# Kernel tuning notes

Measured on AMD Instinct MI355X. Metric: run time of the kernel, lower is better.

Reference implementation:

```python
import jax, jax.numpy as jnp
import numpy as np

DIM = 1024
HEADS = 8
NUM_KEYS = 256
TOPK = 32
D_HEAD = DIM // HEADS
BATCH = 2
SEQ = 2048


def setup_inputs() -> dict:
    key = jax.random.key(0)
    ks = jax.random.split(key, 5)
    x = jax.random.normal(ks[0], (BATCH, SEQ, DIM), jnp.float32)
    # nn.Linear(dim, 2*dim, bias=False): weight (2*dim, dim)
    Wq = jax.random.normal(ks[1], (2 * DIM, DIM), jnp.float32) * (DIM ** -0.5)
    # nn.Parameter(torch.randn(heads, num_keys, 2, d_head))
    keys = jax.random.normal(ks[2], (HEADS, NUM_KEYS, 2, D_HEAD), jnp.float32)
    # nn.Parameter(torch.randn(heads, num_keys**2, d_head))
    values = jax.random.normal(ks[3], (HEADS, NUM_KEYS ** 2, D_HEAD), jnp.float32)
    # nn.Linear(dim, dim): weight (dim, dim), bias (dim,)
    Wo = jax.random.normal(ks[4], (DIM, DIM), jnp.float32) * (DIM ** -0.5)
    bo = jnp.zeros((DIM,), jnp.float32)
    return {"x": x, "Wq": Wq, "keys": keys, "values": values, "Wo": Wo, "bo": bo}


def reference(x, Wq, keys, values, Wo, bo):
    b, t, e = x.shape
    h, dh, k, nk = HEADS, D_HEAD, TOPK, NUM_KEYS
    # to_queries + chunk(2, dim=-1) + stack -> (2, b, t, h, d_head)
    q = x @ Wq.T                                    # (b, t, 2*dim)
    q = q.reshape(b, t, 2, e).transpose(2, 0, 1, 3)  # (2, b, t, dim), matches chunk+stack
    q = q.reshape(2, b, t, h, dh)
    # dual sub-key scores: (b, h, t, 2, num_keys)
    dots = jnp.einsum('pbthd,hnpd->bhtpn', q, keys)
    # top-k over num_keys per sub-key
    scores, indices = jax.lax.top_k(dots, k)         # (b, h, t, 2, k)
    # faithful to source: chunk(2, dim=2) splits the TIME axis
    th = t // 2
    s0, s1 = scores[:, :, :th], scores[:, :, th:]
    i0, i1 = indices[:, :, :th], indices[:, :, th:]
    # Cartesian combination: (b, h, t//2, 2, k, k) -> (b, h, t, k*k)
    all_scores = (s0[..., :, None] + s1[..., None, :]).reshape(b, h, t, k * k)
    all_indices = (i0[..., :, None] * nk + i1[..., None, :]).reshape(b, h, t, k * k)
    # final top-k over the k^2 candidates
    final_scores, final_idx = jax.lax.top_k(all_scores, k)   # (b, h, t, k)
    value_indices = jnp.take_along_axis(all_indices, final_idx, axis=-1)  # (b, h, t, k)
    attn = jax.nn.softmax(final_scores, axis=-1)
    # gather values per head: values (h, nk^2, dh), idx (b, h, t, k) -> (b, h, t, k, dh)
    sel = jax.vmap(lambda v, idx: v[idx], in_axes=(0, 1), out_axes=1)(values, value_indices)
    out = jnp.einsum('bhtk,bhtkd->bhtd', attn, sel)  # weighted sum over top-k
    out = out.transpose(0, 2, 1, 3).reshape(b, t, e)
    return out @ Wo.T + bo
```

## Files before the change

kernel.cpp:

```cpp
#include <hip/hip_runtime.h>

typedef unsigned int u32;
typedef unsigned long long u64;
typedef _Float16 f16;
typedef __attribute__((ext_vector_type(4))) _Float16 f16x4;
typedef __attribute__((ext_vector_type(8))) _Float16 f16x8;
typedef __attribute__((ext_vector_type(4))) float f32x4;
typedef const __attribute__((address_space(1))) void* gp_t;
typedef __attribute__((address_space(3))) void* lp_t;

#define TSEQ 2048

__device__ __forceinline__ u32 f2sort(float f) {
  u32 u = __float_as_uint(f);
  return u ^ ((u32)((int)u >> 31) | 0x80000000u);
}
__device__ __forceinline__ float sort2f(u32 u) {
  u ^= (u & 0x80000000u) ? 0x80000000u : 0xFFFFFFFFu;
  return __uint_as_float(u);
}

__device__ __forceinline__ void glds16(const f16* g, f16* l) {
  __builtin_amdgcn_global_load_lds((gp_t)g, (lp_t)l, 16, 0, 0);
}

__device__ __forceinline__ u32 umax2(u32 a, u32 b) { return a > b ? a : b; }

__device__ __forceinline__ u32 dppmax16(u32 v) {
  u32 t;
  t = (u32)__builtin_amdgcn_update_dpp(0, (int)v, 0x128, 0xF, 0xF, true);
  v = v > t ? v : t;
  t = (u32)__builtin_amdgcn_update_dpp(0, (int)v, 0x124, 0xF, 0xF, true);
  v = v > t ? v : t;
  t = (u32)__builtin_amdgcn_update_dpp(0, (int)v, 0x122, 0xF, 0xF, true);
  v = v > t ? v : t;
  t = (u32)__builtin_amdgcn_update_dpp(0, (int)v, 0x121, 0xF, 0xF, true);
  v = v > t ? v : t;
  return v;
}
__device__ __forceinline__ float dppsum16(float v) {
  float t;
  t = __int_as_float(
      __builtin_amdgcn_update_dpp(0, __float_as_int(v), 0x128, 0xF, 0xF, true));
  v += t;
  t = __int_as_float(
      __builtin_amdgcn_update_dpp(0, __float_as_int(v), 0x124, 0xF, 0xF, true));
  v += t;
  t = __int_as_float(
      __builtin_amdgcn_update_dpp(0, __float_as_int(v), 0x122, 0xF, 0xF, true));
  v += t;
  t = __int_as_float(
      __builtin_amdgcn_update_dpp(0, __float_as_int(v), 0x121, 0xF, 0xF, true));
  v += t;
  return v;
}

__device__ __forceinline__ u32 tree16(const u32* k) {
  u32 t0 = umax2(k[0], k[1]), t1 = umax2(k[2], k[3]);
  u32 t2 = umax2(k[4], k[5]), t3 = umax2(k[6], k[7]);
  u32 t4 = umax2(k[8], k[9]), t5 = umax2(k[10], k[11]);
  u32 t6 = umax2(k[12], k[13]), t7 = umax2(k[14], k[15]);
  t0 = umax2(t0, t1); t2 = umax2(t2, t3);
  t4 = umax2(t4, t5); t6 = umax2(t6, t7);
  return umax2(umax2(t0, t2), umax2(t4, t6));
}

__global__ __launch_bounds__(256) void cvt_all(
    const float* __restrict__ x, const float* __restrict__ wq,
    const float* __restrict__ wo, const float* __restrict__ ky,
    f16* __restrict__ xd, f16* __restrict__ wqd, f16* __restrict__ wod,
    f16* __restrict__ kyd) {
  int g = blockIdx.x * 256 + threadIdx.x;
  const float* s;
  f16* d;
  int off;
  if (g < 1048576)      { s = x;  d = xd;  off = g; }
  else if (g < 1572864) { s = wq; d = wqd; off = g - 1048576; }
  else if (g < 1835008) { s = wo; d = wod; off = g - 1572864; }
  else                  { s = ky; d = kyd; off = g - 1835008; }
  float4 v = ((const float4*)s)[off];
  f16x4 o;
  o[0] = (f16)v.x; o[1] = (f16)v.y; o[2] = (f16)v.z; o[3] = (f16)v.w;
  ((f16x4*)d)[off] = o;
}

template <int BN>
__global__ __launch_bounds__(256) void gemm_f16(
    const f16* __restrict__ A, int lda, const f16* __restrict__ B, int ldb,
    const float* __restrict__ bias, void* __restrict__ Cv, int ldc, int K,
    int c_f16) {
  constexpr int NJ = BN / 32;
  __shared__ f16 As[128 * 32];
  __shared__ f16 Bs[BN * 32];
  const int tid = threadIdx.x;
  const int lane = tid & 63, wave = tid >> 6;
  const int m0 = blockIdx.y << 7, n0 = blockIdx.x * BN;
  const int c0 = wave * 128 + lane, c1 = c0 + 64;
  const int r0 = c0 >> 2, s0 = c0 & 3;
  const int r1 = c1 >> 2, s1 = c1 & 3;
  const int cB = wave * 64 + lane;
  const int rB = cB >> 2, sB = cB & 3;
  const f16* Ab = A + (size_t)m0 * lda;
  const f16* Bb = B + (size_t)n0 * ldb;
  const int fm = lane & 15, fq = lane >> 4, fk = fq << 3;
  const int wm = (wave >> 1) << 6, wn = (wave & 1) * (BN / 2);
  f32x4 acc[4][NJ] = {};
  for (int k0 = 0; k0 < K; k0 += 32) {
    __syncthreads();
    glds16(Ab + (size_t)r0 * lda + k0 + s0 * 8, As + (size_t)c0 * 8 - lane * 8);
    glds16(Ab + (size_t)r1 * lda + k0 + s1 * 8, As + (size_t)c1 * 8 - lane * 8);
    if constexpr (BN == 128) {
      glds16(Bb + (size_t)r0 * ldb + k0 + s0 * 8,
             Bs + (size_t)c0 * 8 - lane * 8);
      glds16(Bb + (size_t)r1 * ldb + k0 + s1 * 8,
             Bs + (size_t)c1 * 8 - lane * 8);
    } else {
      glds16(Bb + (size_t)rB * ldb + k0 + sB * 8,
             Bs + (size_t)cB * 8 - lane * 8);
    }
    __syncthreads();
    f16x8 af[4], bf[NJ];
#pragma unroll
    for (int mi = 0; mi < 4; mi++)
      af[mi] = *(const f16x8*)&As[(wm + mi * 16 + fm) * 32 + fk];
#pragma unroll
    for (int nj = 0; nj < NJ; nj++)
      bf[nj] = *(const f16x8*)&Bs[(wn + nj * 16 + fm) * 32 + fk];
#pragma unroll
    for (int mi = 0; mi < 4; mi++)
#pragma unroll
      for (int nj = 0; nj < NJ; nj++)
        acc[mi][nj] = __builtin_amdgcn_mfma_f32_16x16x32_f16(
            af[mi], bf[nj], acc[mi][nj], 0, 0, 0);
  }
  if (c_f16) {
    f16* C = (f16*)Cv;
#pragma unroll
    for (int mi = 0; mi < 4; mi++)
#pragma unroll
      for (int r = 0; r < 4; r++) {
        int row = m0 + wm + mi * 16 + fq * 4 + r;
        f16* cp = C + (size_t)row * ldc + n0 + wn + fm;
#pragma unroll
        for (int nj = 0; nj < NJ; nj++) cp[nj * 16] = (f16)acc[mi][nj][r];
      }
  } else {
    float* C = (float*)Cv;
    float bb[NJ];
#pragma unroll
    for (int nj = 0; nj < NJ; nj++)
      bb[nj] = bias ? bias[n0 + wn + nj * 16 + fm] : 0.f;
#pragma unroll
    for (int mi = 0; mi < 4; mi++)
#pragma unroll
      for (int r = 0; r < 4; r++) {
        int row = m0 + wm + mi * 16 + fq * 4 + r;
        float* cp = C + (size_t)row * ldc + n0 + wn + fm;
#pragma unroll
        for (int nj = 0; nj < NJ; nj++) cp[nj * 16] = acc[mi][nj][r] + bb[nj];
      }
  }
}

__global__ __launch_bounds__(256) void dots_topk1(
    const f16* __restrict__ Q,
    const f16* __restrict__ keysf,
    float* __restrict__ s1s, int* __restrict__ s1i) {
  __shared__ f16 As[64 * 32];
  __shared__ f16 Bs[256 * 32];
  const int tid = threadIdx.x;
  const int lane = tid & 63, wave = tid >> 6;
  const int z = blockIdx.x;
  const int h = z >> 1, p = z & 1;
  const int m0 = blockIdx.y << 6;
  const f16* Aq = Q + (size_t)m0 * 2048 + p * 1024 + h * 128;
  const f16* Bk = keysf + ((size_t)h * 512 + p) * 128;
  const int cA = wave * 64 + lane;
  const int rA = cA >> 2, sA = cA & 3;
  const int fm = lane & 15, fq = lane >> 4, fk = fq << 3;
  f32x4 acc[16] = {};
  for (int k0 = 0; k0 < 128; k0 += 32) {
    __syncthreads();
    glds16(Aq + (size_t)rA * 2048 + k0 + sA * 8, As + (size_t)cA * 8 - lane * 8);
#pragma unroll
    for (int c = 0; c < 4; c++) {
      int cB = (wave * 4 + c) * 64 + lane;
      int rB = cB >> 2, sB = cB & 3;
      glds16(Bk + (size_t)rB * 256 + k0 + sB * 8,
             Bs + (size_t)cB * 8 - lane * 8);
    }
    __syncthreads();
    f16x8 af = *(const f16x8*)&As[(wave * 16 + fm) * 32 + fk];
#pragma unroll
    for (int j = 0; j < 16; j++) {
      f16x8 bf = *(const f16x8*)&Bs[(j * 16 + fm) * 32 + fk];
      acc[j] = __builtin_amdgcn_mfma_f32_16x16x32_f16(af, bf, acc[j], 0, 0, 0);
    }
  }
#pragma unroll
  for (int rp = 0; rp < 2; rp++) {
    u32 keyA[16], keyB[16];
#pragma unroll
    for (int j = 0; j < 16; j++) {
      keyA[j] = (f2sort(acc[j][2 * rp]) & ~0xFFu) | (u32)((j << 4) | fm);
      keyB[j] = (f2sort(acc[j][2 * rp + 1]) & ~0xFFu) | (u32)((j << 4) | fm);
    }
    u32 g0A = 0, g1A = 0, g0B = 0, g1B = 0;
    for (int it = 0; it < 32; it++) {
      u32 lmA = tree16(keyA);
      u32 lmB = tree16(keyB);
      u32 gmA = dppmax16(lmA);
      u32 gmB = dppmax16(lmB);
#pragma unroll
      for (int j = 0; j < 16; j++) {
        keyA[j] = (keyA[j] == gmA) ? 0u : keyA[j];
        keyB[j] = (keyB[j] == gmB) ? 0u : keyB[j];
      }
      bool sel = (fm == (it & 15));
      if (it < 16) {
        g0A = sel ? gmA : g0A;
        g0B = sel ? gmB : g0B;
      } else {
        g1A = sel ? gmA : g1A;
        g1B = sel ? gmB : g1B;
      }
    }
    int mA = m0 + wave * 16 + (fq << 2) + 2 * rp;
    int bA = mA >> 11, tA = mA & 2047;
    size_t orowA = ((((size_t)(bA * 8 + h)) * TSEQ + tA) * 2 + p) * 32;
    s1s[orowA + fm] = sort2f(g0A & ~0xFFu);
    s1s[orowA + fm + 16] = sort2f(g1A & ~0xFFu);
    s1i[orowA + fm] = (int)(g0A & 0xFFu);
    s1i[orowA + fm + 16] = (int)(g1A & 0xFFu);
    int mB = mA + 1;
    int bB = mB >> 11, tB = mB & 2047;
    size_t orowB = ((((size_t)(bB * 8 + h)) * TSEQ + tB) * 2 + p) * 32;
    s1s[orowB + fm] = sort2f(g0B & ~0xFFu);
    s1s[orowB + fm + 16] = sort2f(g1B & ~0xFFu);
    s1i[orowB + fm] = (int)(g0B & 0xFFu);
    s1i[orowB + fm + 16] = (int)(g1B & 0xFFu);
  }
}

__global__ __launch_bounds__(256) void topk2_gather(
    const float* __restrict__ s1s, const int* __restrict__ s1i,
    const float* __restrict__ valf, f16* __restrict__ headout) {
  __shared__ unsigned short cand[128];
  __shared__ float s0sh[16][32];
  __shared__ float s1sh[16][32];
  __shared__ int i0sh[16][32];
  __shared__ int i1sh[16][32];
  __shared__ int vtab[16][32];
  __shared__ float wtab[16][32];
  const int tid = threadIdx.x;
  if (tid < 128) {
    int c = tid;
    unsigned short enc = 0xFFFF;
    if (c < 119) {
      int rem = c, i = 0;
      for (i = 0; i < 32; i++) {
        int cnt = 32 / (i + 1);
        if (rem < cnt) break;
        rem -= cnt;
      }
      enc = (unsigned short)((i << 5) | rem);
    }
    cand[tid] = enc;
  }
  __syncthreads();
  const int rloc = tid >> 4;
  const int l = tid & 15;
  for (int g = 0; g < 4; g++) {
    const int grp = g * 512 + blockIdx.x;
    const int row = grp * 16 + rloc;
    const int b = row >> 14;
    const int h = (row >> 11) & 7;
    const int t = row & 2047;
    const int tt = t >> 1, p = t & 1;
    size_t rbase = (size_t)(b * 8 + h) * TSEQ;
    size_t base0 = ((rbase + tt) * 2 + p) * 32;
    size_t base1 = ((rbase + tt + 1024) * 2 + p) * 32;
    s0sh[rloc][l] = s1s[base0 + l];
    s0sh[rloc][l + 16] = s1s[base0 + l + 16];
    s1sh[rloc][l] = s1s[base1 + l];
    s1sh[rloc][l + 16] = s1s[base1 + l + 16];
    i0sh[rloc][l] = s1i[base0 + l];
    i0sh[rloc][l + 16] = s1i[base0 + l + 16];
    i1sh[rloc][l] = s1i[base1 + l];
    i1sh[rloc][l + 16] = s1i[base1 + l + 16];
    u32 key[8];
#pragma unroll
    for (int s = 0; s < 8; s++) {
      int c = l + 16 * s;
      unsigned short e = cand[c];
      u32 kk = 0u;
      if (e != 0xFFFF) {
        float v = s0sh[rloc][e >> 5] + s1sh[rloc][e & 31];
        kk = (f2sort(v) & ~0xFFu) | (u32)c;
      }
      key[s] = kk;
    }
    u32 g0 = 0, g1 = 0;
    for (int it = 0; it < 32; it++) {
      u32 t0 = umax2(key[0], key[1]), t1 = umax2(key[2], key[3]);
      u32 t2 = umax2(key[4], key[5]), t3 = umax2(key[6], key[7]);
      u32 lm = umax2(umax2(t0, t1), umax2(t2, t3));
      u32 gm = dppmax16(lm);
#pragma unroll
      for (int s = 0; s < 8; s++) key[s] = (key[s] == gm) ? 0u : key[s];
      bool sel = (l == (it & 15));
      if (it < 16) g0 = sel ? gm : g0;
      else         g1 = sel ? gm : g1;
    }
    float sc0 = sort2f(g0 & ~0xFFu);
    float sc1 = sort2f(g1 & ~0xFFu);
    unsigned short e0c = cand[g0 & 0xFFu];
    unsigned short e1c = cand[g1 & 0xFFu];
    int vidx0 = i0sh[rloc][e0c >> 5] * 256 + i1sh[rloc][e0c & 31];
    int vidx1 = i0sh[rloc][e1c >> 5] * 256 + i1sh[rloc][e1c & 31];
    float mx = __int_as_float(
        __builtin_amdgcn_ds_swizzle(__float_as_int(sc0), 0x010));
    float e0 = __expf(sc0 - mx);
    float e1 = __expf(sc1 - mx);
    float inv = 1.0f / dppsum16(e0 + e1);
    vtab[rloc][l] = vidx0;
    vtab[rloc][l + 16] = vidx1;
    wtab[rloc][l] = e0 * inv;
    wtab[rloc][l + 16] = e1 * inv;
    const float* vb = valf + (((size_t)h) << 23) + (size_t)l * 8;
    float accf[8] = {};
#pragma unroll 8
    for (int k = 0; k < 32; k++) {
      int vi = vtab[rloc][k];
      float wk = wtab[rloc][k];
      const float4* vp = (const float4*)(vb + (size_t)vi * 128);
      float4 v0 = vp[0];
      float4 v1 = vp[1];
      accf[0] += wk * v0.x; accf[1] += wk * v0.y;
      accf[2] += wk * v0.z; accf[3] += wk * v0.w;
      accf[4] += wk * v1.x; accf[5] += wk * v1.y;
      accf[6] += wk * v1.z; accf[7] += wk * v1.w;
    }
    f16x8 o;
#pragma unroll
    for (int j = 0; j < 8; j++) o[j] = (f16)accf[j];
    f16* op = headout + (size_t)(b * TSEQ + t) * 1024 + h * 128 + l * 8;
    *(f16x8*)op = o;
  }
}

extern "C" void kernel_launch(void* const* d_in, const int* in_sizes, int n_in,
                              void* d_out, int out_size, void* d_ws,
                              size_t ws_size, hipStream_t stream) {
  const float* x    = (const float*)d_in[0];
  const float* Wq   = (const float*)d_in[1];
  const float* keys = (const float*)d_in[2];
  const float* vals = (const float*)d_in[3];
  const float* Wo   = (const float*)d_in[4];
  const float* bo   = (const float*)d_in[5];
  float* out = (float*)d_out;
  char* ws = (char*)d_ws;
  f16*   xf   = (f16*)(ws);
  f16*   wqf  = (f16*)(ws + (size_t)(8u << 20));
  f16*   wof  = (f16*)(ws + (size_t)(12u << 20));
  f16*   kyf  = (f16*)(ws + (size_t)(14u << 20));
  f16*   Qf   = (f16*)(ws + (size_t)(16u << 20));
  float* s1s  = (float*)(ws + (size_t)(32u << 20));
  int*   s1i  = (int*)(ws + (size_t)(40u << 20));
  f16*   hof  = (f16*)(ws + (size_t)(48u << 20));

  cvt_all<<<dim3(7680), 256, 0, stream>>>(x, Wq, Wo, keys, xf, wqf, wof, kyf);
  gemm_f16<128><<<dim3(16, 32), 256, 0, stream>>>(xf, 1024, wqf, 1024, nullptr,
                                                  Qf, 2048, 1024, 1);
  dots_topk1<<<dim3(16, 64), 256, 0, stream>>>(Qf, kyf, s1s, s1i);
  topk2_gather<<<dim3(512), 256, 0, stream>>>(s1s, s1i, vals, hof);
  gemm_f16<64><<<dim3(16, 32), 256, 0, stream>>>(hof, 1024, wof, 1024, bo, out,
                                                 1024, 1024, 0);
}
```

Baseline: 535.6 us.

## Fuse query projection GEMM into sub-key dot top-k kernel; flatten gather grid

Measured after the change: 550.6 us. 2.8% more time.

```diff
diff --git a/kernel.cpp b/kernel.cpp
--- a/kernel.cpp
+++ b/kernel.cpp
@@ -162,38 +162,67 @@
   }
 }
 
-__global__ __launch_bounds__(256) void dots_topk1(
-    const f16* __restrict__ Q,
+__global__ __launch_bounds__(256) void qdots_topk1(
+    const f16* __restrict__ xf,
+    const f16* __restrict__ wqf,
     const f16* __restrict__ keysf,
     float* __restrict__ s1s, int* __restrict__ s1i) {
-  __shared__ f16 As[64 * 32];
-  __shared__ f16 Bs[256 * 32];
+  __shared__ f16 Axs[64 * 64];
+  __shared__ f16 Bws[128 * 64];
+  __shared__ f16 Qs[4][64 * 32];
   const int tid = threadIdx.x;
   const int lane = tid & 63, wave = tid >> 6;
   const int z = blockIdx.x;
   const int h = z >> 1, p = z & 1;
   const int m0 = blockIdx.y << 6;
-  const f16* Aq = Q + (size_t)m0 * 2048 + p * 1024 + h * 128;
+  const int nbase = p * 1024 + h * 128;
+  const int fm = lane & 15, fq = lane >> 4, fk = fq << 3;
+  f32x4 accQ[8] = {};
+  for (int k0 = 0; k0 < 1024; k0 += 64) {
+    __syncthreads();
+    {
+      int c = tid;
+      glds16(xf + (size_t)(m0 + (c >> 3)) * 1024 + k0 + (c & 7) * 8,
+             Axs + (size_t)c * 8 - lane * 8);
+      c = tid + 256;
+      glds16(xf + (size_t)(m0 + (c >> 3)) * 1024 + k0 + (c & 7) * 8,
+             Axs + (size_t)c * 8 - lane * 8);
+    }
+#pragma unroll
+    for (int q = 0; q < 4; q++) {
+      int c = tid + 256 * q;
+      glds16(wqf + (size_t)(nbase + (c >> 3)) * 1024 + k0 + (c & 7) * 8,
+             Bws + (size_t)c * 8 - lane * 8);
+    }
+    __syncthreads();
+#pragma unroll
+    for (int s = 0; s < 2; s++) {
+      f16x8 af = *(const f16x8*)&Axs[(wave * 16 + fm) * 64 + s * 32 + fk];
+#pragma unroll
+      for (int j = 0; j < 8; j++) {
+        f16x8 bw = *(const f16x8*)&Bws[(j * 16 + fm) * 64 + s * 32 + fk];
+        accQ[j] =
+            __builtin_amdgcn_mfma_f32_16x16x32_f16(af, bw, accQ[j], 0, 0, 0);
+      }
+    }
+  }
+#pragma unroll
+  for (int j = 0; j < 8; j++) {
+    int pn = j >> 1;
+    int kk = (j & 1) * 16 + fm;
+#pragma unroll
+    for (int r = 0; r < 4; r++)
+      Qs[pn][(wave * 16 + fq * 4 + r) * 32 + kk] = (f16)accQ[j][r];
+  }
+  __syncthreads();
   const f16* Bk = keysf + ((size_t)h * 512 + p) * 128;
-  const int cA = wave * 64 + lane;
-  const int rA = cA >> 2, sA = cA & 3;
-  const int fm = lane & 15, fq = lane >> 4, fk = fq << 3;
   f32x4 acc[16] = {};
+#pragma unroll
   for (int k0 = 0; k0 < 128; k0 += 32) {
-    __syncthreads();
-    glds16(Aq + (size_t)rA * 2048 + k0 + sA * 8, As + (size_t)cA * 8 - lane * 8);
-#pragma unroll
-    for (int c = 0; c < 4; c++) {
-      int cB = (wave * 4 + c) * 64 + lane;
-      int rB = cB >> 2, sB = cB & 3;
-      glds16(Bk + (size_t)rB * 256 + k0 + sB * 8,
-             Bs + (size_t)cB * 8 - lane * 8);
-    }
-    __syncthreads();
-    f16x8 af = *(const f16x8*)&As[(wave * 16 + fm) * 32 + fk];
+    f16x8 af = *(const f16x8*)&Qs[k0 >> 5][(wave * 16 + fm) * 32 + fk];
 #pragma unroll
     for (int j = 0; j < 16; j++) {
-      f16x8 bf = *(const f16x8*)&Bs[(j * 16 + fm) * 32 + fk];
+      f16x8 bf = *(const f16x8*)&Bk[(size_t)(j * 16 + fm) * 256 + k0 + fk];
       acc[j] = __builtin_amdgcn_mfma_f32_16x16x32_f16(af, bf, acc[j], 0, 0, 0);
     }
   }
@@ -267,86 +296,83 @@
     }
     cand[tid] = enc;
   }
-  __syncthreads();
   const int rloc = tid >> 4;
   const int l = tid & 15;
-  for (int g = 0; g < 4; g++) {
-    const int grp = g * 512 + blockIdx.x;
-    const int row = grp * 16 + rloc;
-    const int b = row >> 14;
-    const int h = (row >> 11) & 7;
-    const int t = row & 2047;
-    const int tt = t >> 1, p = t & 1;
-    size_t rbase = (size_t)(b * 8 + h) * TSEQ;
-    size_t base0 = ((rbase + tt) * 2 + p) * 32;
-    size_t base1 = ((rbase + tt + 1024) * 2 + p) * 32;
-    s0sh[rloc][l] = s1s[base0 + l];
-    s0sh[rloc][l + 16] = s1s[base0 + l + 16];
-    s1sh[rloc][l] = s1s[base1 + l];
-    s1sh[rloc][l + 16] = s1s[base1 + l + 16];
-    i0sh[rloc][l] = s1i[base0 + l];
-    i0sh[rloc][l + 16] = s1i[base0 + l + 16];
-    i1sh[rloc][l] = s1i[base1 + l];
-    i1sh[rloc][l + 16] = s1i[base1 + l + 16];
-    u32 key[8];
-#pragma unroll
-    for (int s = 0; s < 8; s++) {
-      int c = l + 16 * s;
-      unsigned short e = cand[c];
-      u32 kk = 0u;
-      if (e != 0xFFFF) {
-        float v = s0sh[rloc][e >> 5] + s1sh[rloc][e & 31];
-        kk = (f2sort(v) & ~0xFFu) | (u32)c;
-      }
-      key[s] = kk;
-    }
-    u32 g0 = 0, g1 = 0;
-    for (int it = 0; it < 32; it++) {
-      u32 t0 = umax2(key[0], key[1]), t1 = umax2(key[2], key[3]);
-      u32 t2 = umax2(key[4], key[5]), t3 = umax2(key[6], key[7]);
-      u32 lm = umax2(umax2(t0, t1), umax2(t2, t3));
-      u32 gm = dppmax16(lm);
-#pragma unroll
-      for (int s = 0; s < 8; s++) key[s] = (key[s] == gm) ? 0u : key[s];
-      bool sel = (l == (it & 15));
-      if (it < 16) g0 = sel ? gm : g0;
-      else         g1 = sel ? gm : g1;
-    }
-    float sc0 = sort2f(g0 & ~0xFFu);
-    float sc1 = sort2f(g1 & ~0xFFu);
-    unsigned short e0c = cand[g0 & 0xFFu];
-    unsigned short e1c = cand[g1 & 0xFFu];
-    int vidx0 = i0sh[rloc][e0c >> 5] * 256 + i1sh[rloc][e0c & 31];
-    int vidx1 = i0sh[rloc][e1c >> 5] * 256 + i1sh[rloc][e1c & 31];
-    float mx = __int_as_float(
-        __builtin_amdgcn_ds_swizzle(__float_as_int(sc0), 0x010));
-    float e0 = __expf(sc0 - mx);
-    float e1 = __expf(sc1 - mx);
-    float inv = 1.0f / dppsum16(e0 + e1);
-    vtab[rloc][l] = vidx0;
-    vtab[rloc][l + 16] = vidx1;
-    wtab[rloc][l] = e0 * inv;
-    wtab[rloc][l + 16] = e1 * inv;
-    const float* vb = valf + (((size_t)h) << 23) + (size_t)l * 8;
-    float accf[8] = {};
+  const int row = blockIdx.x * 16 + rloc;
+  const int b = row >> 14;
+  const int h = (row >> 11) & 7;
+  const int t = row & 2047;
+  const int tt = t >> 1, p = t & 1;
+  size_t rbase = (size_t)(b * 8 + h) * TSEQ;
+  size_t base0 = ((rbase + tt) * 2 + p) * 32;
+  size_t base1 = ((rbase + tt + 1024) * 2 + p) * 32;
+  s0sh[rloc][l] = s1s[base0 + l];
+  s0sh[rloc][l + 16] = s1s[base0 + l + 16];
+  s1sh[rloc][l] = s1s[base1 + l];
+  s1sh[rloc][l + 16] = s1s[base1 + l + 16];
+  i0sh[rloc][l] = s1i[base0 + l];
+  i0sh[rloc][l + 16] = s1i[base0 + l + 16];
+  i1sh[rloc][l] = s1i[base1 + l];
+  i1sh[rloc][l + 16] = s1i[base1 + l + 16];
+  __syncthreads();
+  u32 key[8];
+#pragma unroll
+  for (int s = 0; s < 8; s++) {
+    int c = l + 16 * s;
+    unsigned short e = cand[c];
+    u32 kk = 0u;
+    if (e != 0xFFFF) {
+      float v = s0sh[rloc][e >> 5] + s1sh[rloc][e & 31];
+      kk = (f2sort(v) & ~0xFFu) | (u32)c;
+    }
+    key[s] = kk;
+  }
+  u32 g0 = 0, g1 = 0;
+  for (int it = 0; it < 32; it++) {
+    u32 t0 = umax2(key[0], key[1]), t1 = umax2(key[2], key[3]);
+    u32 t2 = umax2(key[4], key[5]), t3 = umax2(key[6], key[7]);
+    u32 lm = umax2(umax2(t0, t1), umax2(t2, t3));
+    u32 gm = dppmax16(lm);
+#pragma unroll
+    for (int s = 0; s < 8; s++) key[s] = (key[s] == gm) ? 0u : key[s];
+    bool sel = (l == (it & 15));
+    if (it < 16) g0 = sel ? gm : g0;
+    else         g1 = sel ? gm : g1;
+  }
+  float sc0 = sort2f(g0 & ~0xFFu);
+  float sc1 = sort2f(g1 & ~0xFFu);
+  unsigned short e0c = cand[g0 & 0xFFu];
+  unsigned short e1c = cand[g1 & 0xFFu];
+  int vidx0 = i0sh[rloc][e0c >> 5] * 256 + i1sh[rloc][e0c & 31];
+  int vidx1 = i0sh[rloc][e1c >> 5] * 256 + i1sh[rloc][e1c & 31];
+  float mx = __int_as_float(
+      __builtin_amdgcn_ds_swizzle(__float_as_int(sc0), 0x010));
+  float e0 = __expf(sc0 - mx);
+  float e1 = __expf(sc1 - mx);
+  float inv = 1.0f / dppsum16(e0 + e1);
+  vtab[rloc][l] = vidx0;
+  vtab[rloc][l + 16] = vidx1;
+  wtab[rloc][l] = e0 * inv;
+  wtab[rloc][l + 16] = e1 * inv;
+  const float* vb = valf + (((size_t)h) << 23) + (size_t)l * 8;
+  float accf[8] = {};
 #pragma unroll 8
-    for (int k = 0; k < 32; k++) {
-      int vi = vtab[rloc][k];
-      float wk = wtab[rloc][k];
-      const float4* vp = (const float4*)(vb + (size_t)vi * 128);
-      float4 v0 = vp[0];
-      float4 v1 = vp[1];
-      accf[0] += wk * v0.x; accf[1] += wk * v0.y;
-      accf[2] += wk * v0.z; accf[3] += wk * v0.w;
-      accf[4] += wk * v1.x; accf[5] += wk * v1.y;
-      accf[6] += wk * v1.z; accf[7] += wk * v1.w;
-    }
-    f16x8 o;
-#pragma unroll
-    for (int j = 0; j < 8; j++) o[j] = (f16)accf[j];
-    f16* op = headout + (size_t)(b * TSEQ + t) * 1024 + h * 128 + l * 8;
-    *(f16x8*)op = o;
-  }
+  for (int k = 0; k < 32; k++) {
+    int vi = vtab[rloc][k];
+    float wk = wtab[rloc][k];
+    const float4* vp = (const float4*)(vb + (size_t)vi * 128);
+    float4 v0 = vp[0];
+    float4 v1 = vp[1];
+    accf[0] += wk * v0.x; accf[1] += wk * v0.y;
+    accf[2] += wk * v0.z; accf[3] += wk * v0.w;
+    accf[4] += wk * v1.x; accf[5] += wk * v1.y;
+    accf[6] += wk * v1.z; accf[7] += wk * v1.w;
+  }
+  f16x8 o;
+#pragma unroll
+  for (int j = 0; j < 8; j++) o[j] = (f16)accf[j];
+  f16* op = headout + (size_t)(b * TSEQ + t) * 1024 + h * 128 + l * 8;
+  *(f16x8*)op = o;
 }
 
 extern "C" void kernel_launch(void* const* d_in, const int* in_sizes, int n_in,
@@ -364,16 +390,13 @@
   f16*   wqf  = (f16*)(ws + (size_t)(8u << 20));
   f16*   wof  = (f16*)(ws + (size_t)(12u << 20));
   f16*   kyf  = (f16*)(ws + (size_t)(14u << 20));
-  f16*   Qf   = (f16*)(ws + (size_t)(16u << 20));
-  float* s1s  = (float*)(ws + (size_t)(32u << 20));
-  int*   s1i  = (int*)(ws + (size_t)(40u << 20));
-  f16*   hof  = (f16*)(ws + (size_t)(48u << 20));
+  float* s1s  = (float*)(ws + (size_t)(16u << 20));
+  int*   s1i  = (int*)(ws + (size_t)(24u << 20));
+  f16*   hof  = (f16*)(ws + (size_t)(32u << 20));
 
   cvt_all<<<dim3(7680), 256, 0, stream>>>(x, Wq, Wo, keys, xf, wqf, wof, kyf);
-  gemm_f16<128><<<dim3(16, 32), 256, 0, stream>>>(xf, 1024, wqf, 1024, nullptr,
-                                                  Qf, 2048, 1024, 1);
-  dots_topk1<<<dim3(16, 64), 256, 0, stream>>>(Qf, kyf, s1s, s1i);
-  topk2_gather<<<dim3(512), 256, 0, stream>>>(s1s, s1i, vals, hof);
+  qdots_topk1<<<dim3(16, 64), 256, 0, stream>>>(xf, wqf, kyf, s1s, s1i);
+  topk2_gather<<<dim3(32768 / 16), 256, 0, stream>>>(s1s, s1i, vals, hof);
   gemm_f16<64><<<dim3(16, 32), 256, 0, stream>>>(hof, 1024, wof, 1024, bo, out,
                                                  1024, 1024, 0);
 }
```

## Double-buffer LDS tiles in GEMM and dots kernels; flatten topk2 grid

Applied to the files above, without the earlier changes.

After: 515.1 us. 1.04x faster.

```diff
diff --git a/kernel.cpp b/kernel.cpp
--- a/kernel.cpp
+++ b/kernel.cpp
@@ -22,6 +22,17 @@
 
 __device__ __forceinline__ void glds16(const f16* g, f16* l) {
   __builtin_amdgcn_global_load_lds((gp_t)g, (lp_t)l, 16, 0, 0);
+}
+
+template <int N> __device__ __forceinline__ void waitvm() {
+  if constexpr (N == 0) asm volatile("s_waitcnt vmcnt(0)" ::: "memory");
+  else if constexpr (N == 3) asm volatile("s_waitcnt vmcnt(3)" ::: "memory");
+  else if constexpr (N == 4) asm volatile("s_waitcnt vmcnt(4)" ::: "memory");
+  else asm volatile("s_waitcnt vmcnt(5)" ::: "memory");
+}
+__device__ __forceinline__ void barrier_fenced() {
+  __builtin_amdgcn_s_barrier();
+  __builtin_amdgcn_sched_barrier(0);
 }
 
 __device__ __forceinline__ u32 umax2(u32 a, u32 b) { return a > b ? a : b; }
@@ -90,8 +101,9 @@
     const float* __restrict__ bias, void* __restrict__ Cv, int ldc, int K,
     int c_f16) {
   constexpr int NJ = BN / 32;
-  __shared__ f16 As[128 * 32];
-  __shared__ f16 Bs[BN * 32];
+  constexpr int NLD = (BN == 128) ? 4 : 3;
+  __shared__ f16 As[2][128 * 32];
+  __shared__ f16 Bs[2][BN * 32];
   const int tid = threadIdx.x;
   const int lane = tid & 63, wave = tid >> 6;
   const int m0 = blockIdx.y << 7, n0 = blockIdx.x * BN;
@@ -105,33 +117,46 @@
   const int fm = lane & 15, fq = lane >> 4, fk = fq << 3;
   const int wm = (wave >> 1) << 6, wn = (wave & 1) * (BN / 2);
   f32x4 acc[4][NJ] = {};
-  for (int k0 = 0; k0 < K; k0 += 32) {
-    __syncthreads();
-    glds16(Ab + (size_t)r0 * lda + k0 + s0 * 8, As + (size_t)c0 * 8 - lane * 8);
-    glds16(Ab + (size_t)r1 * lda + k0 + s1 * 8, As + (size_t)c1 * 8 - lane * 8);
+  auto stage = [&](int buf, int k0) {
+    glds16(Ab + (size_t)r0 * lda + k0 + s0 * 8,
+           As[buf] + (size_t)c0 * 8 - lane * 8);
+    glds16(Ab + (size_t)r1 * lda + k0 + s1 * 8,
+           As[buf] + (size_t)c1 * 8 - lane * 8);
     if constexpr (BN == 128) {
       glds16(Bb + (size_t)r0 * ldb + k0 + s0 * 8,
-             Bs + (size_t)c0 * 8 - lane * 8);
+             Bs[buf] + (size_t)c0 * 8 - lane * 8);
       glds16(Bb + (size_t)r1 * ldb + k0 + s1 * 8,
-             Bs + (size_t)c1 * 8 - lane * 8);
+             Bs[buf] + (size_t)c1 * 8 - lane * 8);
     } else {
       glds16(Bb + (size_t)rB * ldb + k0 + sB * 8,
-             Bs + (size_t)cB * 8 - lane * 8);
-    }
-    __syncthreads();
+             Bs[buf] + (size_t)cB * 8 - lane * 8);
+    }
+  };
+  const int nt = K >> 5;
+  stage(0, 0);
+  for (int t = 0; t < nt; t++) {
+    const int cur = t & 1;
+    if (t + 1 < nt) {
+      stage(cur ^ 1, (t + 1) << 5);
+      waitvm<NLD>();
+    } else {
+      waitvm<0>();
+    }
+    barrier_fenced();
     f16x8 af[4], bf[NJ];
 #pragma unroll
     for (int mi = 0; mi < 4; mi++)
-      af[mi] = *(const f16x8*)&As[(wm + mi * 16 + fm) * 32 + fk];
+      af[mi] = *(const f16x8*)&As[cur][(wm + mi * 16 + fm) * 32 + fk];
 #pragma unroll
     for (int nj = 0; nj < NJ; nj++)
-      bf[nj] = *(const f16x8*)&Bs[(wn + nj * 16 + fm) * 32 + fk];
+      bf[nj] = *(const f16x8*)&Bs[cur][(wn + nj * 16 + fm) * 32 + fk];
 #pragma unroll
     for (int mi = 0; mi < 4; mi++)
 #pragma unroll
       for (int nj = 0; nj < NJ; nj++)
         acc[mi][nj] = __builtin_amdgcn_mfma_f32_16x16x32_f16(
             af[mi], bf[nj], acc[mi][nj], 0, 0, 0);
+    barrier_fenced();
   }
   if (c_f16) {
     f16* C = (f16*)Cv;
@@ -166,8 +191,8 @@
     const f16* __restrict__ Q,
     const f16* __restrict__ keysf,
     float* __restrict__ s1s, int* __restrict__ s1i) {
-  __shared__ f16 As[64 * 32];
-  __shared__ f16 Bs[256 * 32];
+  __shared__ f16 As[2][64 * 32];
+  __shared__ f16 Bs[2][256 * 32];
   const int tid = threadIdx.x;
   const int lane = tid & 63, wave = tid >> 6;
   const int z = blockIdx.x;
@@ -178,24 +203,35 @@
   const int cA = wave * 64 + lane;
   const int rA = cA >> 2, sA = cA & 3;
   const int fm = lane & 15, fq = lane >> 4, fk = fq << 3;
-  f32x4 acc[16] = {};
-  for (int k0 = 0; k0 < 128; k0 += 32) {
-    __syncthreads();
-    glds16(Aq + (size_t)rA * 2048 + k0 + sA * 8, As + (size_t)cA * 8 - lane * 8);
+  auto stage = [&](int buf, int k0) {
+    glds16(Aq + (size_t)rA * 2048 + k0 + sA * 8,
+           As[buf] + (size_t)cA * 8 - lane * 8);
 #pragma unroll
     for (int c = 0; c < 4; c++) {
       int cB = (wave * 4 + c) * 64 + lane;
       int rB = cB >> 2, sB = cB & 3;
       glds16(Bk + (size_t)rB * 256 + k0 + sB * 8,
-             Bs + (size_t)cB * 8 - lane * 8);
-    }
-    __syncthreads();
-    f16x8 af = *(const f16x8*)&As[(wave * 16 + fm) * 32 + fk];
+             Bs[buf] + (size_t)cB * 8 - lane * 8);
+    }
+  };
+  f32x4 acc[16] = {};
+  stage(0, 0);
+  for (int t = 0; t < 4; t++) {
+    const int cur = t & 1;
+    if (t < 3) {
+      stage(cur ^ 1, (t + 1) << 5);
+      waitvm<5>();
+    } else {
+      waitvm<0>();
+    }
+    barrier_fenced();
+    f16x8 af = *(const f16x8*)&As[cur][(wave * 16 + fm) * 32 + fk];
 #pragma unroll
     for (int j = 0; j < 16; j++) {
-      f16x8 bf = *(const f16x8*)&Bs[(j * 16 + fm) * 32 + fk];
+      f16x8 bf = *(const f16x8*)&Bs[cur][(j * 16 + fm) * 32 + fk];
       acc[j] = __builtin_amdgcn_mfma_f32_16x16x32_f16(af, bf, acc[j], 0, 0, 0);
     }
+    barrier_fenced();
   }
 #pragma unroll
   for (int rp = 0; rp < 2; rp++) {
@@ -267,86 +303,83 @@
     }
     cand[tid] = enc;
   }
-  __syncthreads();
   const int rloc = tid >> 4;
   const int l = tid & 15;
-  for (int g = 0; g < 4; g++) {
-    const int grp = g * 512 + blockIdx.x;
-    const int row = grp * 16 + rloc;
-    const int b = row >> 14;
-    const int h = (row >> 11) & 7;
-    const int t = row & 2047;
-    const int tt = t >> 1, p = t & 1;
-    size_t rbase = (size_t)(b * 8 + h) * TSEQ;
-    size_t base0 = ((rbase + tt) * 2 + p) * 32;
-    size_t base1 = ((rbase + tt + 1024) * 2 + p) * 32;
-    s0sh[rloc][l] = s1s[base0 + l];
-    s0sh[rloc][l + 16] = s1s[base0 + l + 16];
-    s1sh[rloc][l] = s1s[base1 + l];
-    s1sh[rloc][l + 16] = s1s[base1 + l + 16];
-    i0sh[rloc][l] = s1i[base0 + l];
-    i0sh[rloc][l + 16] = s1i[base0 + l + 16];
-    i1sh[rloc][l] = s1i[base1 + l];
-    i1sh[rloc][l + 16] = s1i[base1 + l + 16];
-    u32 key[8];
-#pragma unroll
-    for (int s = 0; s < 8; s++) {
-      int c = l + 16 * s;
-      unsigned short e = cand[c];
-      u32 kk = 0u;
-      if (e != 0xFFFF) {
-        float v = s0sh[rloc][e >> 5] + s1sh[rloc][e & 31];
-        kk = (f2sort(v) & ~0xFFu) | (u32)c;
-      }
-      key[s] = kk;
-    }
-    u32 g0 = 0, g1 = 0;
-    for (int it = 0; it < 32; it++) {
-      u32 t0 = umax2(key[0], key[1]), t1 = umax2(key[2], key[3]);
-      u32 t2 = umax2(key[4], key[5]), t3 = umax2(key[6], key[7]);
-      u32 lm = umax2(umax2(t0, t1), umax2(t2, t3));
-      u32 gm = dppmax16(lm);
-#pragma unroll
-      for (int s = 0; s < 8; s++) key[s] = (key[s] == gm) ? 0u : key[s];
-      bool sel = (l == (it & 15));
-      if (it < 16) g0 = sel ? gm : g0;
-      else         g1 = sel ? gm : g1;
-    }
-    float sc0 = sort2f(g0 & ~0xFFu);
-    float sc1 = sort2f(g1 & ~0xFFu);
-    unsigned short e0c = cand[g0 & 0xFFu];
-    unsigned short e1c = cand[g1 & 0xFFu];
-    int vidx0 = i0sh[rloc][e0c >> 5] * 256 + i1sh[rloc][e0c & 31];
-    int vidx1 = i0sh[rloc][e1c >> 5] * 256 + i1sh[rloc][e1c & 31];
-    float mx = __int_as_float(
-        __builtin_amdgcn_ds_swizzle(__float_as_int(sc0), 0x010));
-    float e0 = __expf(sc0 - mx);
-    float e1 = __expf(sc1 - mx);
-    float inv = 1.0f / dppsum16(e0 + e1);
-    vtab[rloc][l] = vidx0;
-    vtab[rloc][l + 16] = vidx1;
-    wtab[rloc][l] = e0 * inv;
-    wtab[rloc][l + 16] = e1 * inv;
-    const float* vb = valf + (((size_t)h) << 23) + (size_t)l * 8;
-    float accf[8] = {};
+  const int row = blockIdx.x * 16 + rloc;
+  const int b = row >> 14;
+  const int h = (row >> 11) & 7;
+  const int t = row & 2047;
+  const int tt = t >> 1, p = t & 1;
+  size_t rbase = (size_t)(b * 8 + h) * TSEQ;
+  size_t base0 = ((rbase + tt) * 2 + p) * 32;
+  size_t base1 = ((rbase + tt + 1024) * 2 + p) * 32;
+  s0sh[rloc][l] = s1s[base0 + l];
+  s0sh[rloc][l + 16] = s1s[base0 + l + 16];
+  s1sh[rloc][l] = s1s[base1 + l];
+  s1sh[rloc][l + 16] = s1s[base1 + l + 16];
+  i0sh[rloc][l] = s1i[base0 + l];
+  i0sh[rloc][l + 16] = s1i[base0 + l + 16];
+  i1sh[rloc][l] = s1i[base1 + l];
+  i1sh[rloc][l + 16] = s1i[base1 + l + 16];
+  __syncthreads();
+  u32 key[8];
+#pragma unroll
+  for (int s = 0; s < 8; s++) {
+    int c = l + 16 * s;
+    unsigned short e = cand[c];
+    u32 kk = 0u;
+    if (e != 0xFFFF) {
+      float v = s0sh[rloc][e >> 5] + s1sh[rloc][e & 31];
+      kk = (f2sort(v) & ~0xFFu) | (u32)c;
+    }
+    key[s] = kk;
+  }
+  u32 g0 = 0, g1 = 0;
+  for (int it = 0; it < 32; it++) {
+    u32 t0 = umax2(key[0], key[1]), t1 = umax2(key[2], key[3]);
+    u32 t2 = umax2(key[4], key[5]), t3 = umax2(key[6], key[7]);
+    u32 lm = umax2(umax2(t0, t1), umax2(t2, t3));
+    u32 gm = dppmax16(lm);
+#pragma unroll
+    for (int s = 0; s < 8; s++) key[s] = (key[s] == gm) ? 0u : key[s];
+    bool sel = (l == (it & 15));
+    if (it < 16) g0 = sel ? gm : g0;
+    else         g1 = sel ? gm : g1;
+  }
+  float sc0 = sort2f(g0 & ~0xFFu);
+  float sc1 = sort2f(g1 & ~0xFFu);
+  unsigned short e0c = cand[g0 & 0xFFu];
+  unsigned short e1c = cand[g1 & 0xFFu];
+  int vidx0 = i0sh[rloc][e0c >> 5] * 256 + i1sh[rloc][e0c & 31];
+  int vidx1 = i0sh[rloc][e1c >> 5] * 256 + i1sh[rloc][e1c & 31];
+  float mx = __int_as_float(
+      __builtin_amdgcn_ds_swizzle(__float_as_int(sc0), 0x010));
+  float e0 = __expf(sc0 - mx);
+  float e1 = __expf(sc1 - mx);
+  float inv = 1.0f / dppsum16(e0 + e1);
+  vtab[rloc][l] = vidx0;
+  vtab[rloc][l + 16] = vidx1;
+  wtab[rloc][l] = e0 * inv;
+  wtab[rloc][l + 16] = e1 * inv;
+  const float* vb = valf + (((size_t)h) << 23) + (size_t)l * 8;
+  float accf[8] = {};
 #pragma unroll 8
-    for (int k = 0; k < 32; k++) {
-      int vi = vtab[rloc][k];
-      float wk = wtab[rloc][k];
-      const float4* vp = (const float4*)(vb + (size_t)vi * 128);
-      float4 v0 = vp[0];
-      float4 v1 = vp[1];
-      accf[0] += wk * v0.x; accf[1] += wk * v0.y;
-      accf[2] += wk * v0.z; accf[3] += wk * v0.w;
-      accf[4] += wk * v1.x; accf[5] += wk * v1.y;
-      accf[6] += wk * v1.z; accf[7] += wk * v1.w;
-    }
-    f16x8 o;
-#pragma unroll
-    for (int j = 0; j < 8; j++) o[j] = (f16)accf[j];
-    f16* op = headout + (size_t)(b * TSEQ + t) * 1024 + h * 128 + l * 8;
-    *(f16x8*)op = o;
-  }
+  for (int k = 0; k < 32; k++) {
+    int vi = vtab[rloc][k];
+    float wk = wtab[rloc][k];
+    const float4* vp = (const float4*)(vb + (size_t)vi * 128);
+    float4 v0 = vp[0];
+    float4 v1 = vp[1];
+    accf[0] += wk * v0.x; accf[1] += wk * v0.y;
+    accf[2] += wk * v0.z; accf[3] += wk * v0.w;
+    accf[4] += wk * v1.x; accf[5] += wk * v1.y;
+    accf[6] += wk * v1.z; accf[7] += wk * v1.w;
+  }
+  f16x8 o;
+#pragma unroll
+  for (int j = 0; j < 8; j++) o[j] = (f16)accf[j];
+  f16* op = headout + (size_t)(b * TSEQ + t) * 1024 + h * 128 + l * 8;
+  *(f16x8*)op = o;
 }
 
 extern "C" void kernel_launch(void* const* d_in, const int* in_sizes, int n_in,
@@ -373,7 +406,7 @@
   gemm_f16<128><<<dim3(16, 32), 256, 0, stream>>>(xf, 1024, wqf, 1024, nullptr,
                                                   Qf, 2048, 1024, 1);
   dots_topk1<<<dim3(16, 64), 256, 0, stream>>>(Qf, kyf, s1s, s1i);
-  topk2_gather<<<dim3(512), 256, 0, stream>>>(s1s, s1i, vals, hof);
+  topk2_gather<<<dim3(32768 / 16), 256, 0, stream>>>(s1s, s1i, vals, hof);
   gemm_f16<64><<<dim3(16, 32), 256, 0, stream>>>(hof, 1024, wof, 1024, bo, out,
                                                  1024, 1024, 0);
 }
```
